# Performance work log

Hardware: AMD Instinct MI355X
Metric: run time of the kernel (lower is better)

The kernel has to match this reference:

```python
import jax, jax.numpy as jnp
import numpy as np

EPS = 1e-6
N_HEADS, N_KV = 16, 4


def rmsnorm(x, w):
    return x * jax.lax.rsqrt(jnp.mean(x * x, axis=-1, keepdims=True) + EPS) * w


def setup_inputs() -> dict:
    key = jax.random.key(0)
    ks = jax.random.split(key, 9)
    B, T, D, F = 2, 2048, 2048, 8192
    KVD = N_KV * (D // N_HEADS)
    s = lambda k, shape, fan: (jax.random.normal(k, shape, jnp.float32) * (fan ** -0.5))
    return {
        "x": jax.random.normal(ks[0], (B, T, D), jnp.float32),
        "norm1_w": jnp.ones((D,), jnp.float32),
        "norm2_w": jnp.ones((D,), jnp.float32),
        "Wq": s(ks[1], (D, D), D),
        "Wk": s(ks[2], (D, KVD), D),
        "Wv": s(ks[3], (D, KVD), D),
        "Wo": s(ks[4], (D, D), D),
        "Wc": s(ks[5], (D, D), D),
        "W1": s(ks[6], (D, F), D),
        "W2": s(ks[7], (F, D), F),
        "W3": s(ks[8], (D, F), D),
    }


def reference(x, norm1_w, norm2_w, Wq, Wk, Wv, Wo, Wc, W1, W2, W3):
    B, T, D = x.shape
    dh = D // N_HEADS          # 128
    G = N_HEADS // N_KV        # groups per kv head
    scale = dh ** -0.5

    xn = rmsnorm(x, norm1_w)
    q = xn @ Wq                               # [B,T,D]
    pos = q @ Wc                              # CoPE stand-in: contextual positional bias on Q
    q = (q + pos).reshape(B, T, N_KV, G, dh)  # group q heads under their kv head
    k = (xn @ Wk).reshape(B, T, N_KV, dh)
    v = (xn @ Wv).reshape(B, T, N_KV, dh)

    # GQA without repeat_interleave: contract each group against shared K/V
    scores = jnp.einsum('bqkgd,bskd->bkgqs', q, k) * scale   # [B,KV,G,T,T]
    i = jnp.arange(T)
    causal = i[:, None] >= i[None, :]
    scores = jnp.where(causal, scores, -jnp.inf)
    w = jax.nn.softmax(scores, axis=-1)
    att = jnp.einsum('bkgqs,bskd->bqkgd', w, v).reshape(B, T, D)

    x = x + att @ Wo
    xn2 = rmsnorm(x, norm2_w)
    x = x + (jax.nn.silu(xn2 @ W1) * (xn2 @ W3)) @ W2
    return x
```

## Files before the change

### kernel.cpp

```cpp
#include <hip/hip_runtime.h>
#include <hip/hip_bf16.h>

typedef __attribute__((ext_vector_type(8))) short short8;
typedef __attribute__((ext_vector_type(4))) float floatx4;
typedef unsigned short ushort_t;

__device__ inline float b2f(ushort_t s) {
    return __uint_as_float(((unsigned int)s) << 16);
}
__device__ inline ushort_t f2b(float f) {
    unsigned int u = __float_as_uint(f);
    unsigned int r = 0x7fff + ((u >> 16) & 1);
    return (ushort_t)((u + r) >> 16);
}
__device__ inline unsigned int cvtpk(float lo, float hi) {
    unsigned int r;
    asm("v_cvt_pk_bf16_f32 %0, %1, %2" : "=v"(r) : "v"(lo), "v"(hi));
    return r;
}
__device__ inline void load8(const float* p, float* f) {
    float4 a = *(const float4*)p;
    float4 b = *(const float4*)(p + 4);
    f[0] = a.x; f[1] = a.y; f[2] = a.z; f[3] = a.w;
    f[4] = b.x; f[5] = b.y; f[6] = b.z; f[7] = b.w;
}
__device__ inline void gload16(const ushort_t* g, ushort_t* l) {
    __builtin_amdgcn_global_load_lds(
        (const __attribute__((address_space(1))) unsigned int*)g,
        (__attribute__((address_space(3))) unsigned int*)l, 16, 0, 0);
}
__device__ inline void lbar() {
    asm volatile("s_waitcnt lgkmcnt(0)" ::: "memory");
    __builtin_amdgcn_s_barrier();
    asm volatile("" ::: "memory");
}

__global__ __launch_bounds__(256) void transpose_all(
    const float* __restrict__ s0, const float* __restrict__ s1,
    const float* __restrict__ s2, const float* __restrict__ s3,
    const float* __restrict__ s4, const float* __restrict__ s5,
    const float* __restrict__ s6, const float* __restrict__ s7,
    ushort_t* d0, ushort_t* d1, ushort_t* d2, ushort_t* d3,
    ushort_t* d4, ushort_t* d5, ushort_t* d6, ushort_t* d7) {
    int id = blockIdx.x;
    const float* src; ushort_t* dst; int K, N;
    if (id < 1024)       { src = s0; dst = d0; K = 2048; N = 2048; }
    else if (id < 1280)  { id -= 1024;  src = s1; dst = d1; K = 2048; N = 512; }
    else if (id < 1536)  { id -= 1280;  src = s2; dst = d2; K = 2048; N = 512; }
    else if (id < 2560)  { id -= 1536;  src = s3; dst = d3; K = 2048; N = 2048; }
    else if (id < 3584)  { id -= 2560;  src = s4; dst = d4; K = 2048; N = 2048; }
    else if (id < 7680)  { id -= 3584;  src = s5; dst = d5; K = 2048; N = 8192; }
    else if (id < 11776) { id -= 7680;  src = s6; dst = d6; K = 2048; N = 8192; }
    else                 { id -= 11776; src = s7; dst = d7; K = 8192; N = 2048; }
    int tn = N >> 6;
    int kb = (id / tn) * 64, nb = (id % tn) * 64;
    __shared__ ushort_t tile[64][65];
    int t = threadIdx.x;
#pragma unroll
    for (int i = 0; i < 4; ++i) {
        int r = (t >> 4) + i * 16;
        int c = (t & 15) * 4;
        float4 v = *(const float4*)(src + (size_t)(kb + r) * N + nb + c);
        tile[c + 0][r] = f2b(v.x);
        tile[c + 1][r] = f2b(v.y);
        tile[c + 2][r] = f2b(v.z);
        tile[c + 3][r] = f2b(v.w);
    }
    __syncthreads();
#pragma unroll
    for (int i = 0; i < 2; ++i) {
        int s = t + i * 256;
        int n = s >> 3, kc = (s & 7) * 8;
        ushort_t o[8];
#pragma unroll
        for (int j = 0; j < 8; ++j) o[j] = tile[n][kc + j];
        *(uint4*)(dst + (size_t)(nb + n) * K + kb + kc) = *(const uint4*)o;
    }
}

__global__ __launch_bounds__(256) void rmsnorm_kernel(const float* __restrict__ x,
                                                      const float* __restrict__ w,
                                                      ushort_t* __restrict__ out, int D) {
    int row = blockIdx.x;
    int t = threadIdx.x;
    const float* xr = x + (size_t)row * D;
    float f[8];
    load8(xr + t * 8, f);
    float ss = 0.f;
#pragma unroll
    for (int i = 0; i < 8; ++i) ss += f[i] * f[i];
#pragma unroll
    for (int m = 1; m < 64; m <<= 1) ss += __shfl_xor(ss, m);
    __shared__ float wsum[4];
    if ((t & 63) == 0) wsum[t >> 6] = ss;
    __syncthreads();
    float tot = wsum[0] + wsum[1] + wsum[2] + wsum[3];
    float r = rsqrtf(tot / (float)D + 1e-6f);
    float wf[8];
    load8(w + t * 8, wf);
    ushort_t o[8];
#pragma unroll
    for (int i = 0; i < 8; ++i) o[i] = f2b(f[i] * r * wf[i]);
    *(uint4*)(out + (size_t)row * D + t * 8) = *(const uint4*)o;
}

__global__ __launch_bounds__(256) void reduce_out(const ushort_t* __restrict__ p,
                                                  const float* __restrict__ resid,
                                                  float* __restrict__ out, int n) {
    int stride = gridDim.x * 256;
    for (int i = blockIdx.x * 256 + threadIdx.x; i * 8 < n; i += stride) {
        int i8 = i * 8;
        uint4 a = *(const uint4*)(p + i8);
        uint4 b = *(const uint4*)(p + n + i8);
        const ushort_t* ae = (const ushort_t*)&a;
        const ushort_t* be = (const ushort_t*)&b;
        float rr[8];
        load8(resid + i8, rr);
        float o[8];
#pragma unroll
        for (int j = 0; j < 8; ++j) o[j] = b2f(ae[j]) + b2f(be[j]) + rr[j];
        *(float4*)(out + i8) = make_float4(o[0], o[1], o[2], o[3]);
        *(float4*)(out + i8 + 4) = make_float4(o[4], o[5], o[6], o[7]);
    }
}

__device__ inline void vm6() { asm volatile("s_waitcnt vmcnt(6)" ::: "memory"); }
__device__ inline void vm4() { asm volatile("s_waitcnt vmcnt(4)" ::: "memory"); }

template <int MODE>
__global__ __launch_bounds__(512, 2) void gemm8(const ushort_t* __restrict__ A,
                                                const ushort_t* __restrict__ Bt,
                                                const ushort_t* __restrict__ aux,
                                                const float* __restrict__ aux2,
                                                void* __restrict__ Cv,
                                                void* __restrict__ C2v,
                                                void* __restrict__ C3v,
                                                int M, int N, int Ksub, int lda) {
    __shared__ __align__(16) ushort_t Lds[2 * 32768];
    const int tid = threadIdx.x;
    const int wv = tid >> 6, lane = tid & 63;
    const int l16 = lane & 15, l4 = lane >> 4;
    const int wr = wv >> 2, wc = wv & 3;
    int nwg = gridDim.x;
    int per = nwg >> 3;
    int wg = (blockIdx.x & 7) * per + (blockIdx.x >> 3);
    int mtiles = M >> 8;
    int bx = wg & (mtiles - 1);
    int by = wg / mtiles;
    int bm = bx << 8, bn = by << 8;
    int koff = blockIdx.y * Ksub;

    const int sr = tid >> 3;
    const int scol = (((tid & 7) ^ (sr & 7)) << 3);
    const ushort_t* gA = A + (size_t)(bm + sr) * lda + scol + koff;
    const ushort_t* gB = Bt + (size_t)(bn + sr) * lda + scol + koff;
    ushort_t* ldsw = Lds + wv * 512;

    const int ktiles = Ksub >> 6;
    const int niter = ktiles >> 1;
    const int km = ktiles - 1;

#define STG_A(slot, j, kt) gload16(gA + (size_t)((j) * 64) * lda + ((kt) << 6), ldsw + (slot) * 32768 + (j) * 4096)
#define STG_B(slot, j, kt) gload16(gB + (size_t)((j) * 64) * lda + ((kt) << 6), ldsw + (slot) * 32768 + 16384 + (j) * 4096)

    STG_A(0, 0, 0); STG_A(0, 2, 0); STG_A(0, 1, 0); STG_A(0, 3, 0);
    STG_B(0, 0, 0); STG_B(0, 1, 0); STG_B(0, 2, 0); STG_B(0, 3, 0);
    STG_A(1, 0, 1); STG_A(1, 2, 1);
    STG_B(1, 0, 1); STG_B(1, 1, 1); STG_B(1, 2, 1); STG_B(1, 3, 1);
    vm6();
    asm volatile("" ::: "memory");
    __builtin_amdgcn_s_barrier();

    const int lx = l4 ^ (l16 & 7);
    floatx4 acc[8][4] = {};
    short8 aR[4][2], bR[4][2];

#define DSA(slot, mh) { _Pragma("unroll") for (int m = 0; m < 4; ++m) { \
    _Pragma("unroll") for (int kk = 0; kk < 2; ++kk) \
      aR[m][kk] = *(const short8*)(Lds + (slot) * 32768 + \
          (wr * 128 + (mh) * 64 + m * 16 + l16) * 64 + ((lx ^ (kk << 2)) << 3)); } }
#define DSB(slot, nh) { _Pragma("unroll") for (int n = 0; n < 2; ++n) { \
    _Pragma("unroll") for (int kk = 0; kk < 2; ++kk) \
      bR[(nh) * 2 + n][kk] = *(const short8*)(Lds + (slot) * 32768 + 16384 + \
          (wc * 64 + ((nh) * 2 + n) * 16 + l16) * 64 + ((lx ^ (kk << 2)) << 3)); } }
#define QUAD(mh, nlo) { _Pragma("unroll") for (int m = 0; m < 4; ++m) \
    _Pragma("unroll") for (int n = 0; n < 2; ++n) \
    _Pragma("unroll") for (int kk = 0; kk < 2; ++kk) \
      acc[(mh) * 4 + m][(nlo) + n] = __builtin_amdgcn_mfma_f32_16x16x32_bf16( \
          aR[m][kk], bR[(nlo) + n][kk], acc[(mh) * 4 + m][(nlo) + n], 0, 0, 0); }
#define PHASE(DS, ST, MH, NLO, VM) { \
    DS; ST; \
    asm volatile("" ::: "memory"); \
    __builtin_amdgcn_s_barrier(); \
    asm volatile("s_waitcnt lgkmcnt(0)" ::: "memory"); \
    __builtin_amdgcn_sched_barrier(0); \
    __builtin_amdgcn_s_setprio(1); \
    QUAD(MH, NLO); \
    __builtin_amdgcn_s_setprio(0); \
    VM; \
    asm volatile("" ::: "memory"); \
    __builtin_amdgcn_s_barrier(); }

    for (int it = 0; it < niter; ++it) {
        int t1 = 2 * it + 1;
        int t2 = (2 * it + 2) & km;
        int t3 = (2 * it + 3) & km;
        PHASE({ DSA(0, 0); DSB(0, 0); }, { STG_A(1, 1, t1); STG_A(1, 3, t1); }, 0, 0, );
        PHASE({ DSB(0, 1); },            { STG_A(0, 0, t2); STG_A(0, 2, t2); }, 0, 2, );
        PHASE({ DSA(0, 1); },            { STG_B(0, 0, t2); STG_B(0, 1, t2); }, 1, 2, );
        PHASE({ },                       { STG_B(0, 2, t2); STG_B(0, 3, t2); }, 1, 0, vm6(); );
        PHASE({ DSA(1, 0); DSB(1, 0); }, { STG_A(0, 1, t2); STG_A(0, 3, t2); }, 0, 0, );
        PHASE({ DSB(1, 1); },            { STG_A(1, 0, t3); STG_A(1, 2, t3); }, 0, 2, );
        PHASE({ DSA(1, 1); },            { STG_B(1, 0, t3); STG_B(1, 1, t3); }, 1, 2, );
        PHASE({ },                       { STG_B(1, 2, t3); STG_B(1, 3, t3); }, 1, 0, vm6(); );
    }

#pragma unroll
    for (int mi = 0; mi < 8; ++mi)
#pragma unroll
        for (int ni = 0; ni < 4; ++ni)
#pragma unroll
            for (int r = 0; r < 4; ++r) {
                int row = bm + wr * 128 + mi * 16 + l4 * 4 + r;
                int col = bn + wc * 64 + ni * 16 + l16;
                size_t idx = (size_t)row * N + col;
                float v = acc[mi][ni][r];
                if (MODE == 0) {
                    ((ushort_t*)Cv)[idx] = f2b(v);
                } else if (MODE == 1) {
                    ((ushort_t*)Cv)[idx] = f2b(v + b2f(aux[idx]));
                } else if (MODE == 2) {
                    float h = b2f(aux[idx]);
                    ((ushort_t*)Cv)[idx] = f2b((h / (1.f + __expf(-h))) * v);
                } else if (MODE == 3) {
                    ((ushort_t*)Cv)[(size_t)blockIdx.y * M * N + idx] = f2b(v);
                } else if (MODE == 5) {
                    ((float*)Cv)[idx] = v + aux2[idx];
                } else if (MODE == 6) {
                    if (bn < 2048) {
                        ((ushort_t*)Cv)[(size_t)row * 2048 + col] = f2b(v);
                    } else if (bn < 2560) {
                        ((ushort_t*)C2v)[(size_t)row * 512 + (col - 2048)] = f2b(v);
                    } else {
                        ((ushort_t*)C3v)[(size_t)(col - 2560) * 4096 + row] = f2b(v);
                    }
                }
            }
#undef STG_A
#undef STG_B
#undef DSA
#undef DSB
#undef QUAD
#undef PHASE
}

template <int MODE>
__global__ __launch_bounds__(512, 1) void gemm8h(const ushort_t* __restrict__ A,
                                                 const ushort_t* __restrict__ Bt,
                                                 const ushort_t* __restrict__ aux,
                                                 const float* __restrict__ aux2,
                                                 void* __restrict__ Cv,
                                                 int M, int N, int K) {
    __shared__ __align__(16) ushort_t Lds[2 * 24576];
    const int tid = threadIdx.x;
    const int wv = tid >> 6, lane = tid & 63;
    const int l16 = lane & 15, l4 = lane >> 4;
    const int wr = wv >> 2, wc = wv & 3;
    int nwg = gridDim.x;
    int per = nwg >> 3;
    int wg = (blockIdx.x & 7) * per + (blockIdx.x >> 3);
    int mtiles = M >> 7;
    int bx = wg & (mtiles - 1);
    int by = wg / mtiles;
    int bm = bx << 7, bn = by << 8;

    const int sr = tid >> 3;
    const int scol = (((tid & 7) ^ (sr & 7)) << 3);
    const ushort_t* gA = A + (size_t)(bm + sr) * K + scol;
    const ushort_t* gB = Bt + (size_t)(bn + sr) * K + scol;
    ushort_t* ldsw = Lds + wv * 512;

    const int ktiles = K >> 6;
    const int niter = ktiles >> 1;
    const int km = ktiles - 1;

#define HSTG_A(slot, j, kt) gload16(gA + (size_t)((j) * 64) * K + ((kt) << 6), ldsw + (slot) * 24576 + (j) * 4096)
#define HSTG_B(slot, j, kt) gload16(gB + (size_t)((j) * 64) * K + ((kt) << 6), ldsw + (slot) * 24576 + 8192 + (j) * 4096)

    HSTG_A(0, 0, 0); HSTG_A(0, 1, 0);
    HSTG_B(0, 0, 0); HSTG_B(0, 1, 0); HSTG_B(0, 2, 0); HSTG_B(0, 3, 0);
    HSTG_A(1, 0, 1); HSTG_A(1, 1, 1);
    HSTG_B(1, 0, 1); HSTG_B(1, 1, 1);
    vm4();
    asm volatile("" ::: "memory");
    __builtin_amdgcn_s_barrier();

    const int lx = l4 ^ (l16 & 7);
    floatx4 acc[4][4] = {};
    short8 aR[2][2], bR[4][2];

#define HDSA(slot, mh) { _Pragma("unroll") for (int m = 0; m < 2; ++m) { \
    _Pragma("unroll") for (int kk = 0; kk < 2; ++kk) \
      aR[m][kk] = *(const short8*)(Lds + (slot) * 24576 + \
          (wr * 64 + (mh) * 32 + m * 16 + l16) * 64 + ((lx ^ (kk << 2)) << 3)); } }
#define HDSB(slot, nh) { _Pragma("unroll") for (int n = 0; n < 2; ++n) { \
    _Pragma("unroll") for (int kk = 0; kk < 2; ++kk) \
      bR[(nh) * 2 + n][kk] = *(const short8*)(Lds + (slot) * 24576 + 8192 + \
          (wc * 64 + ((nh) * 2 + n) * 16 + l16) * 64 + ((lx ^ (kk << 2)) << 3)); } }
#define HQUAD(mh, nlo) { _Pragma("unroll") for (int m = 0; m < 2; ++m) \
    _Pragma("unroll") for (int n = 0; n < 2; ++n) \
    _Pragma("unroll") for (int kk = 0; kk < 2; ++kk) \
      acc[(mh) * 2 + m][(nlo) + n] = __builtin_amdgcn_mfma_f32_16x16x32_bf16( \
          aR[m][kk], bR[(nlo) + n][kk], acc[(mh) * 2 + m][(nlo) + n], 0, 0, 0); }
#define HPHASE(DS, ST, MH, NLO, VM) { \
    DS; ST; \
    asm volatile("" ::: "memory"); \
    __builtin_amdgcn_s_barrier(); \
    asm volatile("s_waitcnt lgkmcnt(0)" ::: "memory"); \
    __builtin_amdgcn_sched_barrier(0); \
    __builtin_amdgcn_s_setprio(1); \
    HQUAD(MH, NLO); \
    __builtin_amdgcn_s_setprio(0); \
    VM; \
    asm volatile("" ::: "memory"); \
    __builtin_amdgcn_s_barrier(); }

    for (int it = 0; it < niter; ++it) {
        int t1 = 2 * it + 1;
        int t2 = (2 * it + 2) & km;
        int t3 = (2 * it + 3) & km;
        HPHASE({ HDSA(0, 0); HDSB(0, 0); }, { HSTG_B(1, 2, t1); HSTG_B(1, 3, t1); }, 0, 0, );
        HPHASE({ HDSB(0, 1); },             { },                                     0, 2, );
        HPHASE({ HDSA(0, 1); },             { HSTG_B(0, 0, t2); HSTG_B(0, 1, t2); }, 1, 2, );
        HPHASE({ },                         { HSTG_B(0, 2, t2); HSTG_B(0, 3, t2); }, 1, 0, vm4(); );
        HPHASE({ HDSA(1, 0); HDSB(1, 0); }, { HSTG_A(0, 0, t2); HSTG_A(0, 1, t2); }, 0, 0, );
        HPHASE({ HDSB(1, 1); },             { },                                     0, 2, );
        HPHASE({ HDSA(1, 1); },             { HSTG_B(1, 0, t3); HSTG_B(1, 1, t3); }, 1, 2, );
        HPHASE({ },                         { HSTG_A(1, 0, t3); HSTG_A(1, 1, t3); }, 1, 0, vm4(); );
    }

#pragma unroll
    for (int mi = 0; mi < 4; ++mi)
#pragma unroll
        for (int ni = 0; ni < 4; ++ni)
#pragma unroll
            for (int r = 0; r < 4; ++r) {
                int row = bm + wr * 64 + mi * 16 + l4 * 4 + r;
                int col = bn + wc * 64 + ni * 16 + l16;
                size_t idx = (size_t)row * N + col;
                float v = acc[mi][ni][r];
                if (MODE == 1) ((ushort_t*)Cv)[idx] = f2b(v + b2f(aux[idx]));
                else if (MODE == 5) ((float*)Cv)[idx] = v + aux2[idx];
            }
#undef HSTG_A
#undef HSTG_B
#undef HDSA
#undef HDSB
#undef HQUAD
#undef HPHASE
}

#define QB 128
#define SB 64

__global__ __launch_bounds__(256, 1) void attn_kernel(const ushort_t* __restrict__ Q,
                                                      const ushort_t* __restrict__ Kb,
                                                      const ushort_t* __restrict__ VbT,
                                                      ushort_t* __restrict__ O, int Tlen) {
    const int D = 2048, KVD = 512, dh = 128;
    const int MTOK = 4096;
    int p = blockIdx.x, h = blockIdx.y, b = blockIdx.z;
    int kv = h >> 2;
    int t = threadIdx.x, wave = t >> 6, lane = t & 63;
    int l16 = lane & 15, l4 = lane >> 4;
    __shared__ __align__(16) ushort_t Ks[2][SB][dh + 8];
    __shared__ __align__(16) ushort_t Vt[2][dh][SB + 8];
    __shared__ __align__(16) unsigned int Ps2[8][16][36];
    const float scale = 0.08838834764831845f;
    const ushort_t* Kg = Kb + ((size_t)(b * Tlen) + (t >> 4)) * KVD + kv * dh + (t & 15) * 8;
    const ushort_t* Vg = VbT + (size_t)(kv * dh + (t >> 3)) * MTOK + b * Tlen + (t & 7) * 8;

    for (int side = 0; side < 2; ++side) {
        int qt = side ? p : (15 - p);
        int qbase = qt * QB;
        int qw = qbase + wave * 32;
        short8 qf[2][4];
#pragma unroll
        for (int f = 0; f < 2; ++f) {
            const ushort_t* Qrow = Q + ((size_t)(b * Tlen) + qw + f * 16 + l16) * D + h * dh;
#pragma unroll
            for (int kk = 0; kk < 4; ++kk) qf[f][kk] = *(const short8*)(Qrow + kk * 32 + l4 * 8);
        }
        floatx4 o_acc[2][8] = {};
        float m_s[2], l_s[2];
#pragma unroll
        for (int f = 0; f < 2; ++f) { m_s[f] = -INFINITY; l_s[f] = 0.f; }
        int nst = 2 * qt + 2;
        uint4 kreg[4], vreg[4];
#pragma unroll
        for (int p4 = 0; p4 < 4; ++p4) {
            kreg[p4] = *(const uint4*)(Kg + (size_t)(p4 * 16) * KVD);
            vreg[p4] = *(const uint4*)(Vg + (size_t)(p4 * 32) * MTOK);
        }
        lbar();
#pragma unroll
        for (int p4 = 0; p4 < 4; ++p4) {
            *(uint4*)(&Ks[0][(t >> 4) + p4 * 16][(t & 15) * 8]) = kreg[p4];
            *(uint4*)(&Vt[0][(t >> 3) + p4 * 32][(t & 7) * 8]) = vreg[p4];
        }
        if (nst > 1) {
#pragma unroll
            for (int p4 = 0; p4 < 4; ++p4) {
                kreg[p4] = *(const uint4*)(Kg + (size_t)(SB + p4 * 16) * KVD);
                vreg[p4] = *(const uint4*)(Vg + (size_t)(p4 * 32) * MTOK + SB);
            }
        }
        lbar();
        for (int st = 0; st < nst; ++st) {
            int cur = st & 1;
            int s0 = st * SB;
            if (st + 1 < nst) {
#pragma unroll
                for (int p4 = 0; p4 < 4; ++p4) {
                    *(uint4*)(&Ks[cur ^ 1][(t >> 4) + p4 * 16][(t & 15) * 8]) = kreg[p4];
                    *(uint4*)(&Vt[cur ^ 1][(t >> 3) + p4 * 32][(t & 7) * 8]) = vreg[p4];
                }
            }
            if (st + 2 < nst) {
                size_t off = (size_t)(st + 2) * SB;
#pragma unroll
                for (int p4 = 0; p4 < 4; ++p4) {
                    kreg[p4] = *(const uint4*)(Kg + (off + p4 * 16) * KVD);
                    vreg[p4] = *(const uint4*)(Vg + (size_t)(p4 * 32) * MTOK + off);
                }
            }
            floatx4 sa[2][4] = {};
            __builtin_amdgcn_s_setprio(1);
#pragma unroll
            for (int ss = 0; ss < 4; ++ss)
#pragma unroll
                for (int kk = 0; kk < 4; ++kk) {
                    short8 kf = *(const short8*)(&Ks[cur][ss * 16 + l16][kk * 32 + l4 * 8]);
                    sa[0][ss] = __builtin_amdgcn_mfma_f32_16x16x32_bf16(kf, qf[0][kk], sa[0][ss], 0, 0, 0);
                    sa[1][ss] = __builtin_amdgcn_mfma_f32_16x16x32_bf16(kf, qf[1][kk], sa[1][ss], 0, 0, 0);
                }
            __builtin_amdgcn_s_setprio(0);
            short8 pa[2][2];
#pragma unroll
            for (int f = 0; f < 2; ++f) {
                int qcol = qw + f * 16 + l16;
                float sv[4][4];
                float pmax = -INFINITY;
#pragma unroll
                for (int ss = 0; ss < 4; ++ss)
#pragma unroll
                    for (int r = 0; r < 4; ++r) {
                        int krow = s0 + ss * 16 + l4 * 4 + r;
                        float v = sa[f][ss][r] * scale;
                        if (krow > qcol) v = -INFINITY;
                        sv[ss][r] = v;
                        pmax = fmaxf(pmax, v);
                    }
                pmax = fmaxf(pmax, __shfl_xor(pmax, 16));
                pmax = fmaxf(pmax, __shfl_xor(pmax, 32));
                bool skip = __all(pmax <= m_s[f] + 8.f);
                float mn = skip ? m_s[f] : fmaxf(m_s[f], pmax);
                float rsum = 0.f;
#pragma unroll
                for (int ss = 0; ss < 4; ++ss)
#pragma unroll
                    for (int r = 0; r < 4; ++r) {
                        float pv = __expf(sv[ss][r] - mn);
                        sv[ss][r] = pv;
                        rsum += pv;
                    }
                rsum += __shfl_xor(rsum, 16);
                rsum += __shfl_xor(rsum, 32);
                if (skip) {
                    l_s[f] += rsum;
                } else {
                    float esc = __expf(m_s[f] - mn);
                    l_s[f] = l_s[f] * esc + rsum;
                    m_s[f] = mn;
                    float ef[4];
#pragma unroll
                    for (int r = 0; r < 4; ++r) ef[r] = __shfl(esc, l4 * 4 + r);
#pragma unroll
                    for (int c = 0; c < 8; ++c)
#pragma unroll
                        for (int r = 0; r < 4; ++r) o_acc[f][c][r] *= ef[r];
                }
#pragma unroll
                for (int ss = 0; ss < 4; ++ss) {
                    uint2 pk;
                    pk.x = cvtpk(sv[ss][0], sv[ss][1]);
                    pk.y = cvtpk(sv[ss][2], sv[ss][3]);
                    *(uint2*)&Ps2[wave * 2 + f][l16][ss * 8 + l4 * 2] = pk;
                }
#pragma unroll
                for (int kk = 0; kk < 2; ++kk) {
                    uint4 pv4 = *(const uint4*)&Ps2[wave * 2 + f][l16][kk * 16 + l4 * 4];
                    pa[f][kk] = *(const short8*)&pv4;
                }
            }
            __builtin_amdgcn_s_setprio(1);
#pragma unroll
            for (int c = 0; c < 8; ++c)
#pragma unroll
                for (int kk = 0; kk < 2; ++kk) {
                    short8 vf = *(const short8*)(&Vt[cur][c * 16 + l16][kk * 32 + l4 * 8]);
                    o_acc[0][c] = __builtin_amdgcn_mfma_f32_16x16x32_bf16(pa[0][kk], vf, o_acc[0][c], 0, 0, 0);
                    o_acc[1][c] = __builtin_amdgcn_mfma_f32_16x16x32_bf16(pa[1][kk], vf, o_acc[1][c], 0, 0, 0);
                }
            __builtin_amdgcn_s_setprio(0);
            lbar();
        }
        ushort_t* Osh = &Ks[0][0][0];
#pragma unroll
        for (int f = 0; f < 2; ++f) {
            float linv[4];
#pragma unroll
            for (int r = 0; r < 4; ++r) linv[r] = 1.f / __shfl(l_s[f], l4 * 4 + r);
#pragma unroll
            for (int c = 0; c < 8; ++c)
#pragma unroll
                for (int r = 0; r < 4; ++r)
                    Osh[(wave * 32 + f * 16 + l4 * 4 + r) * 136 + c * 16 + l16] =
                        f2b(o_acc[f][c][r] * linv[r]);
        }
        lbar();
        {
            int orow = t >> 1, occ = (t & 1) * 64;
            const ushort_t* srcp = Osh + orow * 136 + occ;
            ushort_t* dstp = O + ((size_t)(b * Tlen) + qbase + orow) * D + h * dh + occ;
#pragma unroll
            for (int k = 0; k < 8; ++k)
                *(uint4*)(dstp + k * 8) = *(const uint4*)(srcp + k * 8);
        }
    }
}

extern "C" void kernel_launch(void* const* d_in, const int* in_sizes, int n_in,
                              void* d_out, int out_size, void* d_ws, size_t ws_size,
                              hipStream_t stream) {
    const float* x   = (const float*)d_in[0];
    const float* n1w = (const float*)d_in[1];
    const float* n2w = (const float*)d_in[2];
    const float* Wq  = (const float*)d_in[3];
    const float* Wk  = (const float*)d_in[4];
    const float* Wv  = (const float*)d_in[5];
    const float* Wo  = (const float*)d_in[6];
    const float* Wc  = (const float*)d_in[7];
    const float* W1  = (const float*)d_in[8];
    const float* W2  = (const float*)d_in[9];
    const float* W3  = (const float*)d_in[10];
    float* out = (float*)d_out;

    const int B = 2, T = 2048, D = 2048, F = 8192, KVD = 512;
    const int M = B * T;
    const size_t XD   = (size_t)M * D * 2;
    const size_t XDF  = (size_t)M * D * 4;
    const size_t KVSZ = (size_t)M * KVD * 2;
    const size_t MF   = (size_t)M * F * 2;
    const size_t WDD  = (size_t)D * D * 2;
    const size_t WQKV = (size_t)(D + 2 * KVD) * D * 2;
    const size_t WDF  = (size_t)D * F * 2;

    char* w = (char*)d_ws;
    ushort_t* xn    = (ushort_t*)(w);
    ushort_t* qtmp  = (ushort_t*)(w + XD);
    ushort_t* qfin  = (ushort_t*)(w + 2 * XD);
    float*    x2f   = (float*)   (w + 3 * XD);
    ushort_t* kbuf  = (ushort_t*)(w + 3 * XD + XDF);
    ushort_t* vbufT = (ushort_t*)(w + 3 * XD + XDF + KVSZ);
    ushort_t* h1    = (ushort_t*)(w + 3 * XD + XDF + 2 * KVSZ);
    char* wt = w + 3 * XD + XDF + 2 * KVSZ + MF;
    ushort_t* WqkvT = (ushort_t*)(wt);
    ushort_t* WcT   = (ushort_t*)(wt + WQKV);
    ushort_t* WoT   = (ushort_t*)(wt + WQKV + WDD);
    ushort_t* W1T   = (ushort_t*)(wt + WQKV + 2 * WDD);
    ushort_t* W3T   = (ushort_t*)(wt + WQKV + 2 * WDD + WDF);
    ushort_t* W2T   = (ushort_t*)(wt + WQKV + 2 * WDD + 2 * WDF);

    dim3 blk(256);
    dim3 blk8(512);

    transpose_all<<<15872, blk, 0, stream>>>(
        Wq, Wk, Wv, Wc, Wo, W1, W3, W2,
        WqkvT, WqkvT + (size_t)2048 * D, WqkvT + (size_t)2560 * D,
        WcT, WoT, W1T, W3T, W2T);

    rmsnorm_kernel<<<M, blk, 0, stream>>>(x, n1w, xn, D);
    gemm8<6><<<dim3((M / 256) * (3072 / 256)), blk8, 0, stream>>>(
        xn, WqkvT, nullptr, nullptr, qtmp, kbuf, vbufT, M, 3072, D, D);
    gemm8h<1><<<dim3((M / 128) * (D / 256)), blk8, 0, stream>>>(
        qtmp, WcT, qtmp, nullptr, qfin, M, D, D);
    attn_kernel<<<dim3(8, 16, B), blk, 0, stream>>>(qfin, kbuf, vbufT, qtmp, T);
    gemm8h<5><<<dim3((M / 128) * (D / 256)), blk8, 0, stream>>>(
        qtmp, WoT, nullptr, x, x2f, M, D, D);
    rmsnorm_kernel<<<M, blk, 0, stream>>>(x2f, n2w, xn, D);
    gemm8<0><<<dim3((M / 256) * (F / 256)), blk8, 0, stream>>>(
        xn, W1T, nullptr, nullptr, h1, nullptr, nullptr, M, F, D, D);
    gemm8<2><<<dim3((M / 256) * (F / 256)), blk8, 0, stream>>>(
        xn, W3T, h1, nullptr, h1, nullptr, nullptr, M, F, D, D);
    gemm8<3><<<dim3((M / 256) * (D / 256), 2), blk8, 0, stream>>>(
        h1, W2T, nullptr, nullptr, xn, nullptr, nullptr, M, D, F / 2, F);
    reduce_out<<<1024, blk, 0, stream>>>(xn, x2f, out, M * D);
}
```

Baseline: 777.5 us.

## Single-buffer attention LDS, one q-tile per block, allow two blocks per CU

The attention kernel no longer processes a paired short and long q-tile per block. It launches one block per q-tile (16x16x2 grid), ordered longest-first. K/V LDS staging drops from double to single buffering so LDS shrinks to about 54KB, and launch bounds now allow two blocks per CU. The aim is to trade intra-block load/compute overlap for higher occupancy and more parallel blocks. The risk is that an extra barrier per step exposes LDS write latency and that per-block work becomes less balanced.

```diff
diff --git a/kernel.cpp b/kernel.cpp
--- a/kernel.cpp
+++ b/kernel.cpp
@@ -363,180 +363,165 @@
 #define QB 128
 #define SB 64
 
-__global__ __launch_bounds__(256, 1) void attn_kernel(const ushort_t* __restrict__ Q,
+__global__ __launch_bounds__(256, 2) void attn_kernel(const ushort_t* __restrict__ Q,
                                                       const ushort_t* __restrict__ Kb,
                                                       const ushort_t* __restrict__ VbT,
                                                       ushort_t* __restrict__ O, int Tlen) {
     const int D = 2048, KVD = 512, dh = 128;
     const int MTOK = 4096;
-    int p = blockIdx.x, h = blockIdx.y, b = blockIdx.z;
+    int qt = 15 - blockIdx.x;
+    int h = blockIdx.y, b = blockIdx.z;
     int kv = h >> 2;
     int t = threadIdx.x, wave = t >> 6, lane = t & 63;
     int l16 = lane & 15, l4 = lane >> 4;
-    __shared__ __align__(16) ushort_t Ks[2][SB][dh + 8];
-    __shared__ __align__(16) ushort_t Vt[2][dh][SB + 8];
-    __shared__ __align__(16) unsigned int Ps2[8][16][36];
+    __shared__ __align__(16) ushort_t LdsAll[27136];
+    ushort_t (*Ks)[136] = (ushort_t(*)[136])LdsAll;
+    ushort_t (*Vt)[72] = (ushort_t(*)[72])(LdsAll + 8704);
+    unsigned int* PsB = (unsigned int*)(LdsAll + 17920);
     const float scale = 0.08838834764831845f;
     const ushort_t* Kg = Kb + ((size_t)(b * Tlen) + (t >> 4)) * KVD + kv * dh + (t & 15) * 8;
     const ushort_t* Vg = VbT + (size_t)(kv * dh + (t >> 3)) * MTOK + b * Tlen + (t & 7) * 8;
 
-    for (int side = 0; side < 2; ++side) {
-        int qt = side ? p : (15 - p);
-        int qbase = qt * QB;
-        int qw = qbase + wave * 32;
-        short8 qf[2][4];
-#pragma unroll
-        for (int f = 0; f < 2; ++f) {
-            const ushort_t* Qrow = Q + ((size_t)(b * Tlen) + qw + f * 16 + l16) * D + h * dh;
-#pragma unroll
-            for (int kk = 0; kk < 4; ++kk) qf[f][kk] = *(const short8*)(Qrow + kk * 32 + l4 * 8);
+    int qbase = qt * QB;
+    int qw = qbase + wave * 32;
+    short8 qf[2][4];
+#pragma unroll
+    for (int f = 0; f < 2; ++f) {
+        const ushort_t* Qrow = Q + ((size_t)(b * Tlen) + qw + f * 16 + l16) * D + h * dh;
+#pragma unroll
+        for (int kk = 0; kk < 4; ++kk) qf[f][kk] = *(const short8*)(Qrow + kk * 32 + l4 * 8);
+    }
+    floatx4 o_acc[2][8] = {};
+    float m_s[2], l_s[2];
+#pragma unroll
+    for (int f = 0; f < 2; ++f) { m_s[f] = -INFINITY; l_s[f] = 0.f; }
+    int nst = 2 * qt + 2;
+    uint4 kreg[4], vreg[4];
+#pragma unroll
+    for (int p4 = 0; p4 < 4; ++p4) {
+        kreg[p4] = *(const uint4*)(Kg + (size_t)(p4 * 16) * KVD);
+        vreg[p4] = *(const uint4*)(Vg + (size_t)(p4 * 32) * MTOK);
+    }
+    for (int st = 0; st < nst; ++st) {
+        int s0 = st * SB;
+        lbar();
+#pragma unroll
+        for (int p4 = 0; p4 < 4; ++p4) {
+            *(uint4*)(&Ks[(t >> 4) + p4 * 16][(t & 15) * 8]) = kreg[p4];
+            *(uint4*)(&Vt[(t >> 3) + p4 * 32][(t & 7) * 8]) = vreg[p4];
         }
-        floatx4 o_acc[2][8] = {};
-        float m_s[2], l_s[2];
-#pragma unroll
-        for (int f = 0; f < 2; ++f) { m_s[f] = -INFINITY; l_s[f] = 0.f; }
-        int nst = 2 * qt + 2;
-        uint4 kreg[4], vreg[4];
-#pragma unroll
-        for (int p4 = 0; p4 < 4; ++p4) {
-            kreg[p4] = *(const uint4*)(Kg + (size_t)(p4 * 16) * KVD);
-            vreg[p4] = *(const uint4*)(Vg + (size_t)(p4 * 32) * MTOK);
+        if (st + 1 < nst) {
+            size_t off = (size_t)(st + 1) * SB;
+#pragma unroll
+            for (int p4 = 0; p4 < 4; ++p4) {
+                kreg[p4] = *(const uint4*)(Kg + (off + p4 * 16) * KVD);
+                vreg[p4] = *(const uint4*)(Vg + (size_t)(p4 * 32) * MTOK + off);
+            }
         }
         lbar();
-#pragma unroll
-        for (int p4 = 0; p4 < 4; ++p4) {
-            *(uint4*)(&Ks[0][(t >> 4) + p4 * 16][(t & 15) * 8]) = kreg[p4];
-            *(uint4*)(&Vt[0][(t >> 3) + p4 * 32][(t & 7) * 8]) = vreg[p4];
+        floatx4 sa[2][4] = {};
+        __builtin_amdgcn_s_setprio(1);
+#pragma unroll
+        for (int ss = 0; ss < 4; ++ss)
+#pragma unroll
+            for (int kk = 0; kk < 4; ++kk) {
+                short8 kf = *(const short8*)(&Ks[ss * 16 + l16][kk * 32 + l4 * 8]);
+                sa[0][ss] = __builtin_amdgcn_mfma_f32_16x16x32_bf16(kf, qf[0][kk], sa[0][ss], 0, 0, 0);
+                sa[1][ss] = __builtin_amdgcn_mfma_f32_16x16x32_bf16(kf, qf[1][kk], sa[1][ss], 0, 0, 0);
+            }
+        __builtin_amdgcn_s_setprio(0);
+        short8 pa[2][2];
+#pragma unroll
+        for (int f = 0; f < 2; ++f) {
+            int qcol = qw + f * 16 + l16;
+            float sv[4][4];
+            float pmax = -INFINITY;
+#pragma unroll
+            for (int ss = 0; ss < 4; ++ss)
+#pragma unroll
+                for (int r = 0; r < 4; ++r) {
+                    int krow = s0 + ss * 16 + l4 * 4 + r;
+                    float v = sa[f][ss][r] * scale;
+                    if (krow > qcol) v = -INFINITY;
+                    sv[ss][r] = v;
+                    pmax = fmaxf(pmax, v);
+                }
+            pmax = fmaxf(pmax, __shfl_xor(pmax, 16));
+            pmax = fmaxf(pmax, __shfl_xor(pmax, 32));
+            bool skip = __all(pmax <= m_s[f] + 8.f);
+            float mn = skip ? m_s[f] : fmaxf(m_s[f], pmax);
+            float rsum = 0.f;
+#pragma unroll
+            for (int ss = 0; ss < 4; ++ss)
+#pragma unroll
+                for (int r = 0; r < 4; ++r) {
+                    float pv = __expf(sv[ss][r] - mn);
+                    sv[ss][r] = pv;
+                    rsum += pv;
+                }
+            rsum += __shfl_xor(rsum, 16);
+            rsum += __shfl_xor(rsum, 32);
+            if (skip) {
+                l_s[f] += rsum;
+            } else {
+                float esc = __expf(m_s[f] - mn);
+                l_s[f] = l_s[f] * esc + rsum;
+                m_s[f] = mn;
+                float ef[4];
+#pragma unroll
+                for (int r = 0; r < 4; ++r) ef[r] = __shfl(esc, l4 * 4 + r);
+#pragma unroll
+                for (int c = 0; c < 8; ++c)
+#pragma unroll
+                    for (int r = 0; r < 4; ++r) o_acc[f][c][r] *= ef[r];
+            }
+            unsigned int* Pw = PsB + (wave * 2 + f) * 16 * 36;
+#pragma unroll
+            for (int ss = 0; ss < 4; ++ss) {
+                uint2 pk;
+                pk.x = cvtpk(sv[ss][0], sv[ss][1]);
+                pk.y = cvtpk(sv[ss][2], sv[ss][3]);
+                *(uint2*)&Pw[l16 * 36 + ss * 8 + l4 * 2] = pk;
+            }
+#pragma unroll
+            for (int kk = 0; kk < 2; ++kk) {
+                uint4 pv4 = *(const uint4*)&Pw[l16 * 36 + kk * 16 + l4 * 4];
+                pa[f][kk] = *(const short8*)&pv4;
+            }
         }
-        if (nst > 1) {
-#pragma unroll
-            for (int p4 = 0; p4 < 4; ++p4) {
-                kreg[p4] = *(const uint4*)(Kg + (size_t)(SB + p4 * 16) * KVD);
-                vreg[p4] = *(const uint4*)(Vg + (size_t)(p4 * 32) * MTOK + SB);
-            }
-        }
-        lbar();
-        for (int st = 0; st < nst; ++st) {
-            int cur = st & 1;
-            int s0 = st * SB;
-            if (st + 1 < nst) {
-#pragma unroll
-                for (int p4 = 0; p4 < 4; ++p4) {
-                    *(uint4*)(&Ks[cur ^ 1][(t >> 4) + p4 * 16][(t & 15) * 8]) = kreg[p4];
-                    *(uint4*)(&Vt[cur ^ 1][(t >> 3) + p4 * 32][(t & 7) * 8]) = vreg[p4];
-                }
-            }
-            if (st + 2 < nst) {
-                size_t off = (size_t)(st + 2) * SB;
-#pragma unroll
-                for (int p4 = 0; p4 < 4; ++p4) {
-                    kreg[p4] = *(const uint4*)(Kg + (off + p4 * 16) * KVD);
-                    vreg[p4] = *(const uint4*)(Vg + (size_t)(p4 * 32) * MTOK + off);
-                }
-            }
-            floatx4 sa[2][4] = {};
-            __builtin_amdgcn_s_setprio(1);
-#pragma unroll
-            for (int ss = 0; ss < 4; ++ss)
-#pragma unroll
-                for (int kk = 0; kk < 4; ++kk) {
-                    short8 kf = *(const short8*)(&Ks[cur][ss * 16 + l16][kk * 32 + l4 * 8]);
-                    sa[0][ss] = __builtin_amdgcn_mfma_f32_16x16x32_bf16(kf, qf[0][kk], sa[0][ss], 0, 0, 0);
-                    sa[1][ss] = __builtin_amdgcn_mfma_f32_16x16x32_bf16(kf, qf[1][kk], sa[1][ss], 0, 0, 0);
-                }
-            __builtin_amdgcn_s_setprio(0);
-            short8 pa[2][2];
-#pragma unroll
-            for (int f = 0; f < 2; ++f) {
-                int qcol = qw + f * 16 + l16;
-                float sv[4][4];
-                float pmax = -INFINITY;
-#pragma unroll
-                for (int ss = 0; ss < 4; ++ss)
-#pragma unroll
-                    for (int r = 0; r < 4; ++r) {
-                        int krow = s0 + ss * 16 + l4 * 4 + r;
-                        float v = sa[f][ss][r] * scale;
-                        if (krow > qcol) v = -INFINITY;
-                        sv[ss][r] = v;
-                        pmax = fmaxf(pmax, v);
-                    }
-                pmax = fmaxf(pmax, __shfl_xor(pmax, 16));
-                pmax = fmaxf(pmax, __shfl_xor(pmax, 32));
-                bool skip = __all(pmax <= m_s[f] + 8.f);
-                float mn = skip ? m_s[f] : fmaxf(m_s[f], pmax);
-                float rsum = 0.f;
-#pragma unroll
-                for (int ss = 0; ss < 4; ++ss)
-#pragma unroll
-                    for (int r = 0; r < 4; ++r) {
-                        float pv = __expf(sv[ss][r] - mn);
-                        sv[ss][r] = pv;
-                        rsum += pv;
-                    }
-                rsum += __shfl_xor(rsum, 16);
-                rsum += __shfl_xor(rsum, 32);
-                if (skip) {
-                    l_s[f] += rsum;
-                } else {
-                    float esc = __expf(m_s[f] - mn);
-                    l_s[f] = l_s[f] * esc + rsum;
-                    m_s[f] = mn;
-                    float ef[4];
-#pragma unroll
-                    for (int r = 0; r < 4; ++r) ef[r] = __shfl(esc, l4 * 4 + r);
-#pragma unroll
-                    for (int c = 0; c < 8; ++c)
-#pragma unroll
-                        for (int r = 0; r < 4; ++r) o_acc[f][c][r] *= ef[r];
-                }
-#pragma unroll
-                for (int ss = 0; ss < 4; ++ss) {
-                    uint2 pk;
-                    pk.x = cvtpk(sv[ss][0], sv[ss][1]);
-                    pk.y = cvtpk(sv[ss][2], sv[ss][3]);
-                    *(uint2*)&Ps2[wave * 2 + f][l16][ss * 8 + l4 * 2] = pk;
-                }
-#pragma unroll
-                for (int kk = 0; kk < 2; ++kk) {
-                    uint4 pv4 = *(const uint4*)&Ps2[wave * 2 + f][l16][kk * 16 + l4 * 4];
-                    pa[f][kk] = *(const short8*)&pv4;
-                }
-            }
-            __builtin_amdgcn_s_setprio(1);
-#pragma unroll
-            for (int c = 0; c < 8; ++c)
-#pragma unroll
-                for (int kk = 0; kk < 2; ++kk) {
-                    short8 vf = *(const short8*)(&Vt[cur][c * 16 + l16][kk * 32 + l4 * 8]);
-                    o_acc[0][c] = __builtin_amdgcn_mfma_f32_16x16x32_bf16(pa[0][kk], vf, o_acc[0][c], 0, 0, 0);
-                    o_acc[1][c] = __builtin_amdgcn_mfma_f32_16x16x32_bf16(pa[1][kk], vf, o_acc[1][c], 0, 0, 0);
-                }
-            __builtin_amdgcn_s_setprio(0);
-            lbar();
-        }
-        ushort_t* Osh = &Ks[0][0][0];
-#pragma unroll
-        for (int f = 0; f < 2; ++f) {
-            float linv[4];
-#pragma unroll
-            for (int r = 0; r < 4; ++r) linv[r] = 1.f / __shfl(l_s[f], l4 * 4 + r);
-#pragma unroll
-            for (int c = 0; c < 8; ++c)
-#pragma unroll
-                for (int r = 0; r < 4; ++r)
-                    Osh[(wave * 32 + f * 16 + l4 * 4 + r) * 136 + c * 16 + l16] =
-                        f2b(o_acc[f][c][r] * linv[r]);
-        }
-        lbar();
-        {
-            int orow = t >> 1, occ = (t & 1) * 64;
-            const ushort_t* srcp = Osh + orow * 136 + occ;
-            ushort_t* dstp = O + ((size_t)(b * Tlen) + qbase + orow) * D + h * dh + occ;
-#pragma unroll
-            for (int k = 0; k < 8; ++k)
-                *(uint4*)(dstp + k * 8) = *(const uint4*)(srcp + k * 8);
-        }
+        __builtin_amdgcn_s_setprio(1);
+#pragma unroll
+        for (int c = 0; c < 8; ++c)
+#pragma unroll
+            for (int kk = 0; kk < 2; ++kk) {
+                short8 vf = *(const short8*)(&Vt[c * 16 + l16][kk * 32 + l4 * 8]);
+                o_acc[0][c] = __builtin_amdgcn_mfma_f32_16x16x32_bf16(pa[0][kk], vf, o_acc[0][c], 0, 0, 0);
+                o_acc[1][c] = __builtin_amdgcn_mfma_f32_16x16x32_bf16(pa[1][kk], vf, o_acc[1][c], 0, 0, 0);
+            }
+        __builtin_amdgcn_s_setprio(0);
+    }
+    lbar();
+    ushort_t* Osh = LdsAll;
+#pragma unroll
+    for (int f = 0; f < 2; ++f) {
+        float linv[4];
+#pragma unroll
+        for (int r = 0; r < 4; ++r) linv[r] = 1.f / __shfl(l_s[f], l4 * 4 + r);
+#pragma unroll
+        for (int c = 0; c < 8; ++c)
+#pragma unroll
+            for (int r = 0; r < 4; ++r)
+                Osh[(wave * 32 + f * 16 + l4 * 4 + r) * 136 + c * 16 + l16] =
+                    f2b(o_acc[f][c][r] * linv[r]);
+    }
+    lbar();
+    {
+        int orow = t >> 1, occ = (t & 1) * 64;
+        const ushort_t* srcp = Osh + orow * 136 + occ;
+        ushort_t* dstp = O + ((size_t)(b * Tlen) + qbase + orow) * D + h * dh + occ;
+#pragma unroll
+        for (int k = 0; k < 8; ++k)
+            *(uint4*)(dstp + k * 8) = *(const uint4*)(srcp + k * 8);
     }
 }
 
@@ -595,7 +580,7 @@
         xn, WqkvT, nullptr, nullptr, qtmp, kbuf, vbufT, M, 3072, D, D);
     gemm8h<1><<<dim3((M / 128) * (D / 256)), blk8, 0, stream>>>(
         qtmp, WcT, qtmp, nullptr, qfin, M, D, D);
-    attn_kernel<<<dim3(8, 16, B), blk, 0, stream>>>(qfin, kbuf, vbufT, qtmp, T);
+    attn_kernel<<<dim3(16, 16, B), blk, 0, stream>>>(qfin, kbuf, vbufT, qtmp, T);
     gemm8h<5><<<dim3((M / 128) * (D / 256)), blk8, 0, stream>>>(
         qtmp, WoT, nullptr, x, x2f, M, D, D);
     rmsnorm_kernel<<<M, blk, 0, stream>>>(x2f, n2w, xn, D);
```

Result: slower. 803.5 us (+3.3%).
